# Kernel tuning notes

Hardware: AMD Instinct MI355X
Metric: run time of the kernel (lower is better)

## Reference

```python
import jax, jax.numpy as jnp
import numpy as np

ALPHA, BETA, GAMMA = 2.0, 2.0, 1.0
EPS = 1e-8  # torch F.cosine_similarity eps
B, T, D = 64, 1024, 256


def setup_inputs() -> dict:
    key = jax.random.key(0)
    k1, k2, k3 = jax.random.split(key, 3)
    f_v = jax.random.normal(k1, (B, T, D), dtype=jnp.float32)
    f_a = jax.random.normal(k2, (B, T, D), dtype=jnp.float32)
    labels = jax.random.randint(k3, (B,), 0, 2, dtype=jnp.int64)
    return {"f_v": f_v, "f_a": f_a, "labels": labels}


def _normalize(x):
    n = jnp.sqrt(jnp.sum(x * x, axis=-1, keepdims=True))
    return x / jnp.maximum(n, EPS)


def reference(f_v, f_a, labels):
    b, t, _ = f_v.shape
    vn = _normalize(f_v)  # [B,T,D]
    an = _normalize(f_a)  # [B,T,D]

    # --- per-timestep aligned-pair term ---
    cos_bt = jnp.sum(vn * an, axis=-1)  # [B,T] cosine sim
    d_bt = 1.0 - cos_bt                  # cosine distance
    pos_mask = (labels == 0).astype(f_v.dtype)[:, None]  # [B,1]
    neg_mask = 1.0 - pos_mask
    loss_pos = ALPHA * jnp.sum(d_bt * pos_mask)
    cnt_pos = jnp.sum(pos_mask) * t
    loss_neg = BETA * jnp.sum((1.0 - d_bt) * neg_mask)  # (1-d) == cos
    cnt_neg = jnp.sum(neg_mask) * t

    # --- cross-sample term: for i != j, (1 - mean_t d_ij) = mean_t cos(v_i_t, a_j_t) ---
    cross_cos = jnp.einsum('itd,jtd->ij', vn, an) / t  # [B,B] mean over T
    offdiag = 1.0 - jnp.eye(b, dtype=f_v.dtype)
    loss_neg = loss_neg + GAMMA * jnp.sum(cross_cos * offdiag)
    cnt_neg = cnt_neg + b * (b - 1)

    loss = jnp.where(cnt_pos > 0, loss_pos / jnp.maximum(cnt_pos, 1.0), 0.0)
    loss = loss + jnp.where(cnt_neg > 0, loss_neg / jnp.maximum(cnt_neg, 1.0), 0.0)
    return loss
```

## Files before the change

### kernel.cpp

```cpp
#include <hip/hip_runtime.h>

constexpr int Bn = 64;
constexpr int Tn = 1024;
constexpr int Dn = 256;

constexpr int TPB  = 256;
constexpr int NBLK = Tn;
constexpr int CH   = 32;
constexpr int NCH  = Dn / CH;
constexpr int NBIN = 64;

using short8 = __attribute__((ext_vector_type(8))) short;
using f32x16 = __attribute__((ext_vector_type(16))) float;

__device__ __forceinline__ float dot4(const float4& a, const float4& b) {
    return a.x * b.x + a.y * b.y + a.z * b.z + a.w * b.w;
}

__device__ __forceinline__ unsigned int bfbits(float x) {
    unsigned int u = __builtin_bit_cast(unsigned int, x);
    return (u + 0x7FFFu + ((u >> 16) & 1u)) >> 16;
}
__device__ __forceinline__ unsigned int pack_bf2(float lo, float hi) {
    return bfbits(lo) | (bfbits(hi) << 16);
}

__device__ __forceinline__ void gload16(const float* g, float* l) {
    __builtin_amdgcn_global_load_lds(
        (const __attribute__((address_space(1))) void*)g,
        (__attribute__((address_space(3))) void*)l,
        16, 0, 0);
}

#define VM_BARRIER(N) do {                                      \
    asm volatile("s_waitcnt vmcnt(" #N ")" ::: "memory");       \
    __builtin_amdgcn_sched_barrier(0);                          \
    __builtin_amdgcn_s_barrier();                               \
    __builtin_amdgcn_sched_barrier(0);                          \
} while (0)

#define RD_BARRIER() do {                                       \
    asm volatile("s_waitcnt lgkmcnt(0)" ::: "memory");          \
    __builtin_amdgcn_sched_barrier(0);                          \
    __builtin_amdgcn_s_barrier();                               \
    __builtin_amdgcn_sched_barrier(0);                          \
} while (0)

__global__ __launch_bounds__(TPB, 4)
void cmfm_main(const float* __restrict__ fv, const float* __restrict__ fa,
               const int* __restrict__ labels, float* __restrict__ acc)
{
    __shared__ __align__(16) float Vb[2][Bn * CH];
    __shared__ __align__(16) float Ab[2][Bn * CH];
    __shared__ float rvs[Bn], ras[Bn];
    __shared__ float wred[3][TPB / 64];

    const int tid  = threadIdx.x;
    const int lane = tid & 63;
    const int wave = tid >> 6;
    const int t    = blockIdx.x;

    const int i0   = (wave >> 1) * 32;
    const int j0   = (wave & 1) * 32;
    const int mrow = lane & 31;
    const int half = lane >> 5;
    const bool diag = (i0 == j0);

    const int rV = i0 + mrow;
    const int rA = j0 + mrow;
    const unsigned vbase = (unsigned)rV * CH;
    const unsigned abase = (unsigned)rA * CH;
    const int kV = rV & 7;
    const int kA = rA & 7;

    const int sr0 = (tid >> 3);
    const int su0 = (tid & 7);

    f32x16 C;
    #pragma unroll
    for (int r = 0; r < 16; ++r) C[r] = 0.f;

    float sqv = 0.f, sqa = 0.f, dva = 0.f;

    #define STAGE(c, b) do {                                                        \
        _Pragma("unroll")                                                           \
        for (int n = 0; n < 2; ++n) {                                               \
            const int r  = n * 32 + sr0;                                            \
            const int u  = su0 ^ (r & 7);                                           \
            const size_t goff = ((size_t)r * Tn + t) * Dn + (c) * CH + u * 4;       \
            gload16(fv + goff, &Vb[b][n * 1024 + tid * 4]);                         \
            gload16(fa + goff, &Ab[b][n * 1024 + tid * 4]);                         \
        }                                                                           \
    } while (0)

    STAGE(0, 0);
    STAGE(1, 1);

    #pragma unroll
    for (int c = 0; c < NCH; ++c) {
        const int b = c & 1;
        if (c < NCH - 1) { VM_BARRIER(4); }
        else            { VM_BARRIER(0); }

        #pragma unroll
        for (int s = 0; s < 2; ++s) {
            const int us = 4 * s + 2 * half;
            const float4 v0 = *reinterpret_cast<const float4*>(&Vb[b][vbase + (((us    ) ^ kV) << 2)]);
            const float4 v1 = *reinterpret_cast<const float4*>(&Vb[b][vbase + (((us + 1) ^ kV) << 2)]);
            const float4 a0 = *reinterpret_cast<const float4*>(&Ab[b][abase + (((us    ) ^ kA) << 2)]);
            const float4 a1 = *reinterpret_cast<const float4*>(&Ab[b][abase + (((us + 1) ^ kA) << 2)]);

            if (diag) {
                sqv += dot4(v0, v0) + dot4(v1, v1);
                sqa += dot4(a0, a0) + dot4(a1, a1);
                dva += dot4(v0, a0) + dot4(v1, a1);
            }

            union { short8 s8; uint4 u4; } av, bv;
            av.u4.x = pack_bf2(v0.x, v0.y); av.u4.y = pack_bf2(v0.z, v0.w);
            av.u4.z = pack_bf2(v1.x, v1.y); av.u4.w = pack_bf2(v1.z, v1.w);
            bv.u4.x = pack_bf2(a0.x, a0.y); bv.u4.y = pack_bf2(a0.z, a0.w);
            bv.u4.z = pack_bf2(a1.x, a1.y); bv.u4.w = pack_bf2(a1.z, a1.w);
            C = __builtin_amdgcn_mfma_f32_32x32x16_bf16(av.s8, bv.s8, C, 0, 0, 0);
        }

        RD_BARRIER();
        if (c + 2 < NCH) STAGE(c + 2, b);
    }
    #undef STAGE

    float pos = 0.f, neg = 0.f;
    if (diag) {
        sqv += __shfl_xor(sqv, 32);
        sqa += __shfl_xor(sqa, 32);
        dva += __shfl_xor(dva, 32);
        const float rv = 1.f / fmaxf(sqrtf(sqv), 1e-8f);
        const float ra = 1.f / fmaxf(sqrtf(sqa), 1e-8f);
        if (half == 0) {
            rvs[rV] = rv;
            ras[rV] = ra;
            const float cosd = dva * rv * ra;
            if (labels[rV] == 0) pos = 1.f - cosd;
            else                 neg = cosd;
        }
    }
    RD_BARRIER();

    const float raj = ras[j0 + mrow];
    float od = 0.f;
    #pragma unroll
    for (int r = 0; r < 16; ++r) {
        const int ri = (r & 3) + 8 * (r >> 2) + 4 * half;
        float cc = C[r];
        if (diag && ri == mrow) cc = 0.f;
        od += rvs[i0 + ri] * raj * cc;
    }

    #pragma unroll
    for (int off = 1; off < 64; off <<= 1) {
        pos += __shfl_xor(pos, off);
        neg += __shfl_xor(neg, off);
        od  += __shfl_xor(od, off);
    }
    if (lane == 0) { wred[0][wave] = pos; wred[1][wave] = neg; wred[2][wave] = od; }
    __syncthreads();
    if (tid == 0) {
        float p = 0.f, n = 0.f, o = 0.f;
        #pragma unroll
        for (int w = 0; w < TPB / 64; ++w) { p += wred[0][w]; n += wred[1][w]; o += wred[2][w]; }
        float* bin = acc + (size_t)(blockIdx.x & (NBIN - 1)) * 4;
        atomicAdd(bin + 0, p);
        atomicAdd(bin + 1, n);
        atomicAdd(bin + 2, o);
    }
}

__global__ void cmfm_final(const int* __restrict__ labels, const float* __restrict__ acc,
                           float* __restrict__ out) {
    const int l = threadIdx.x;
    float p = acc[l * 4 + 0];
    float n = acc[l * 4 + 1];
    float o = acc[l * 4 + 2];
    float npf = (labels[l] == 0) ? 1.f : 0.f;
    #pragma unroll
    for (int off = 1; off < 64; off <<= 1) {
        p += __shfl_xor(p, off);
        n += __shfl_xor(n, off);
        o += __shfl_xor(o, off);
        npf += __shfl_xor(npf, off);
    }
    if (l == 0) {
        const int np = (int)(npf + 0.5f);
        const float cnt_pos = (float)np * (float)Tn;
        const float cnt_neg = (float)(Bn - np) * (float)Tn + (float)Bn * (float)(Bn - 1);
        float loss = 0.f;
        if (np > 0) loss += 2.0f * p / cnt_pos;
        loss += (2.0f * n + 1.0f * o / (float)Tn) / cnt_neg;
        out[0] = loss;
    }
}

extern "C" void kernel_launch(void* const* d_in, const int* in_sizes, int n_in,
                              void* d_out, int out_size, void* d_ws, size_t ws_size,
                              hipStream_t stream) {
    const float* fv     = (const float*)d_in[0];
    const float* fa     = (const float*)d_in[1];
    const int*   labels = (const int*)d_in[2];
    float* acc = (float*)d_ws;
    float* out = (float*)d_out;

    hipMemsetAsync(acc, 0, NBIN * 4 * sizeof(float), stream);
    cmfm_main<<<NBLK, TPB, 0, stream>>>(fv, fa, labels, acc);
    cmfm_final<<<1, 64, 0, stream>>>(labels, acc, out);
}
```

Baseline: 153.5 us.

## Use 4-buffer ring with 16-wide chunks and single barrier per step

Halves the D-chunk width and replaces the double-buffered V/A arrays with a four-slot ring buffer. Each slot interleaves V and A rows and uses a new XOR swizzle, and loads are prefetched three chunks ahead. The read-side barrier after each chunk is removed because the ring depth keeps the slot being overwritten from colliding with the one being read. This gives more loads in flight and fewer barriers, but doubles the number of loop iterations and adds more per-iteration barrier waits on smaller chunks.

```diff
diff --git a/kernel.cpp b/kernel.cpp
--- a/kernel.cpp
+++ b/kernel.cpp
@@ -6,7 +6,7 @@
 
 constexpr int TPB  = 256;
 constexpr int NBLK = Tn;
-constexpr int CH   = 32;
+constexpr int CH   = 16;
 constexpr int NCH  = Dn / CH;
 constexpr int NBIN = 64;
 
@@ -28,30 +28,21 @@
 __device__ __forceinline__ void gload16(const float* g, float* l) {
     __builtin_amdgcn_global_load_lds(
         (const __attribute__((address_space(1))) void*)g,
-        (__attribute__((address_space(3))) void*)l,
-        16, 0, 0);
-}
-
-#define VM_BARRIER(N) do {                                      \
+        (__attribute__((address_space(3))) void*)l, 16, 0, 0);
+}
+
+#define SYNC_AFTER_VMWAIT(N) do {                               \
     asm volatile("s_waitcnt vmcnt(" #N ")" ::: "memory");       \
     __builtin_amdgcn_sched_barrier(0);                          \
     __builtin_amdgcn_s_barrier();                               \
     __builtin_amdgcn_sched_barrier(0);                          \
 } while (0)
 
-#define RD_BARRIER() do {                                       \
-    asm volatile("s_waitcnt lgkmcnt(0)" ::: "memory");          \
-    __builtin_amdgcn_sched_barrier(0);                          \
-    __builtin_amdgcn_s_barrier();                               \
-    __builtin_amdgcn_sched_barrier(0);                          \
-} while (0)
-
 __global__ __launch_bounds__(TPB, 4)
 void cmfm_main(const float* __restrict__ fv, const float* __restrict__ fa,
                const int* __restrict__ labels, float* __restrict__ acc)
 {
-    __shared__ __align__(16) float Vb[2][Bn * CH];
-    __shared__ __align__(16) float Ab[2][Bn * CH];
+    __shared__ __align__(16) float buf[4][2048];
     __shared__ float rvs[Bn], ras[Bn];
     __shared__ float wred[3][TPB / 64];
 
@@ -66,15 +57,30 @@
     const int half = lane >> 5;
     const bool diag = (i0 == j0);
 
-    const int rV = i0 + mrow;
-    const int rA = j0 + mrow;
-    const unsigned vbase = (unsigned)rV * CH;
-    const unsigned abase = (unsigned)rA * CH;
-    const int kV = rV & 7;
-    const int kA = rA & 7;
-
-    const int sr0 = (tid >> 3);
-    const int su0 = (tid & 7);
+    const float* sp0; const float* sp1;
+    {
+        #pragma unroll
+        for (int n = 0; n < 2; ++n) {
+            const int u    = n * 256 + tid;
+            const int line = u >> 4;
+            const int pos  = u & 15;
+            const int l    = pos ^ (line & 15);
+            const int r    = 2 * line + (l >> 3);
+            const int cat  = l & 7;
+            const float* base = (cat < 4) ? fv : fa;
+            const float* p = base + ((size_t)r * Tn + t) * Dn + (cat & 3) * 4;
+            if (n == 0) sp0 = p; else sp1 = p;
+        }
+    }
+
+    const int rV = i0 + mrow, rA = j0 + mrow;
+    const int lnV = rV >> 1, lnA = rA >> 1;
+    const int lV = 8 * (rV & 1) + 2 * half;
+    const int lA = 8 * (rA & 1) + 4 + 2 * half;
+    const int uV0 = lnV * 16 + ((lV    ) ^ (lnV & 15));
+    const int uV1 = lnV * 16 + ((lV + 1) ^ (lnV & 15));
+    const int uA0 = lnA * 16 + ((lA    ) ^ (lnA & 15));
+    const int uA1 = lnA * 16 + ((lA + 1) ^ (lnA & 15));
 
     f32x16 C;
     #pragma unroll
@@ -82,50 +88,40 @@
 
     float sqv = 0.f, sqa = 0.f, dva = 0.f;
 
-    #define STAGE(c, b) do {                                                        \
-        _Pragma("unroll")                                                           \
-        for (int n = 0; n < 2; ++n) {                                               \
-            const int r  = n * 32 + sr0;                                            \
-            const int u  = su0 ^ (r & 7);                                           \
-            const size_t goff = ((size_t)r * Tn + t) * Dn + (c) * CH + u * 4;       \
-            gload16(fv + goff, &Vb[b][n * 1024 + tid * 4]);                         \
-            gload16(fa + goff, &Ab[b][n * 1024 + tid * 4]);                         \
-        }                                                                           \
+    #define STAGE(c) do {                                       \
+        float* dst = &buf[(c) & 3][0];                          \
+        gload16(sp0 + (c) * CH, dst + tid * 4);                 \
+        gload16(sp1 + (c) * CH, dst + 1024 + tid * 4);          \
     } while (0)
 
-    STAGE(0, 0);
-    STAGE(1, 1);
+    STAGE(0); STAGE(1); STAGE(2);
 
     #pragma unroll
     for (int c = 0; c < NCH; ++c) {
-        const int b = c & 1;
-        if (c < NCH - 1) { VM_BARRIER(4); }
-        else            { VM_BARRIER(0); }
-
-        #pragma unroll
-        for (int s = 0; s < 2; ++s) {
-            const int us = 4 * s + 2 * half;
-            const float4 v0 = *reinterpret_cast<const float4*>(&Vb[b][vbase + (((us    ) ^ kV) << 2)]);
-            const float4 v1 = *reinterpret_cast<const float4*>(&Vb[b][vbase + (((us + 1) ^ kV) << 2)]);
-            const float4 a0 = *reinterpret_cast<const float4*>(&Ab[b][abase + (((us    ) ^ kA) << 2)]);
-            const float4 a1 = *reinterpret_cast<const float4*>(&Ab[b][abase + (((us + 1) ^ kA) << 2)]);
-
-            if (diag) {
-                sqv += dot4(v0, v0) + dot4(v1, v1);
-                sqa += dot4(a0, a0) + dot4(a1, a1);
-                dva += dot4(v0, a0) + dot4(v1, a1);
-            }
-
-            union { short8 s8; uint4 u4; } av, bv;
-            av.u4.x = pack_bf2(v0.x, v0.y); av.u4.y = pack_bf2(v0.z, v0.w);
-            av.u4.z = pack_bf2(v1.x, v1.y); av.u4.w = pack_bf2(v1.z, v1.w);
-            bv.u4.x = pack_bf2(a0.x, a0.y); bv.u4.y = pack_bf2(a0.z, a0.w);
-            bv.u4.z = pack_bf2(a1.x, a1.y); bv.u4.w = pack_bf2(a1.z, a1.w);
-            C = __builtin_amdgcn_mfma_f32_32x32x16_bf16(av.s8, bv.s8, C, 0, 0, 0);
+        if      (c <  NCH - 2) SYNC_AFTER_VMWAIT(4);
+        else if (c == NCH - 2) SYNC_AFTER_VMWAIT(2);
+        else                   SYNC_AFTER_VMWAIT(0);
+
+        const float* rb = &buf[c & 3][0];
+        const float4 v0 = *reinterpret_cast<const float4*>(rb + uV0 * 4);
+        const float4 v1 = *reinterpret_cast<const float4*>(rb + uV1 * 4);
+        const float4 a0 = *reinterpret_cast<const float4*>(rb + uA0 * 4);
+        const float4 a1 = *reinterpret_cast<const float4*>(rb + uA1 * 4);
+
+        if (diag) {
+            sqv += dot4(v0, v0) + dot4(v1, v1);
+            sqa += dot4(a0, a0) + dot4(a1, a1);
+            dva += dot4(v0, a0) + dot4(v1, a1);
         }
 
-        RD_BARRIER();
-        if (c + 2 < NCH) STAGE(c + 2, b);
+        union { short8 s8; uint4 u4; } av, bv;
+        av.u4.x = pack_bf2(v0.x, v0.y); av.u4.y = pack_bf2(v0.z, v0.w);
+        av.u4.z = pack_bf2(v1.x, v1.y); av.u4.w = pack_bf2(v1.z, v1.w);
+        bv.u4.x = pack_bf2(a0.x, a0.y); bv.u4.y = pack_bf2(a0.z, a0.w);
+        bv.u4.z = pack_bf2(a1.x, a1.y); bv.u4.w = pack_bf2(a1.z, a1.w);
+        C = __builtin_amdgcn_mfma_f32_32x32x16_bf16(av.s8, bv.s8, C, 0, 0, 0);
+
+        if (c + 3 < NCH) STAGE(c + 3);
     }
     #undef STAGE
 
@@ -144,7 +140,7 @@
             else                 neg = cosd;
         }
     }
-    RD_BARRIER();
+    __syncthreads();
 
     const float raj = ras[j0 + mrow];
     float od = 0.f;
```

Result: no change. 156.1 us (+1.7%).
